# Kernel tuning notes

Measured on AMD Instinct MI355X. Metric: run time of the kernel, lower is better.

## Reference

```python
import jax, jax.numpy as jnp
import numpy as np


def setup_inputs() -> dict:
    key = jax.random.key(0)
    ks = jax.random.split(key, 10)
    B, C, D, H, W = 2, 512, 8, 32, 32
    Ck = C // 4  # shared KV head dim (and fixed query dim per intended MQA math)
    s = 0.02
    return {
        "x": jax.random.normal(ks[0], (B, C, D, H, W), dtype=jnp.float32),
        "Wq": jax.random.normal(ks[1], (Ck, C), dtype=jnp.float32) * s,
        "bq": jnp.zeros((Ck,), dtype=jnp.float32),
        "Wk": jax.random.normal(ks[2], (Ck, C), dtype=jnp.float32) * s,
        "bk": jnp.zeros((Ck,), dtype=jnp.float32),
        "Wv": jax.random.normal(ks[3], (Ck, C), dtype=jnp.float32) * s,
        "bv": jnp.zeros((Ck,), dtype=jnp.float32),
        "Wo": jax.random.normal(ks[4], (C, C), dtype=jnp.float32) * s,
        "bo": jnp.zeros((C,), dtype=jnp.float32),
    }


def reference(x, Wq, bq, Wk, bk, Wv, bv, Wo, bo):
    B, C, D, H, W = x.shape
    N = D * H * W
    Ck = Wk.shape[0]  # C // 4
    xf = x.reshape(B, C, N)  # flatten spatial dims -> sequence axis
    # 1x1 Conv3d == per-voxel linear projection over channels
    q = jnp.einsum('oc,bcn->bno', Wq, xf) + bq  # [B, N, Ck]
    k = jnp.einsum('oc,bcn->bno', Wk, xf) + bk  # [B, N, Ck]
    v = jnp.einsum('oc,bcn->bno', Wv, xf) + bv  # [B, N, Ck]
    scale = jnp.asarray(Ck, x.dtype) ** -0.5
    attn = jax.nn.softmax(jnp.einsum('bnc,bmc->bnm', q, k) * scale, axis=-1)  # [B, N, N]
    out = jnp.einsum('bnm,bmc->bnc', attn, v)  # [B, N, Ck]
    out = jnp.tile(out, (1, 1, 4))  # repeat(1,1,4) -> [B, N, C]
    out = jnp.einsum('oc,bnc->bon', Wo, out) + bo[None, :, None]  # [B, C, N]
    return out.reshape(B, C, D, H, W) + x
```

## Files before the change

kernel.cpp:

```cpp
#include <hip/hip_runtime.h>
#include <hip/hip_bf16.h>

typedef __bf16 bf16;
typedef __bf16 bf16x8 __attribute__((ext_vector_type(8)));
typedef __bf16 bf16x4 __attribute__((ext_vector_type(4)));
typedef float  f32x4  __attribute__((ext_vector_type(4)));
typedef float  f32x16 __attribute__((ext_vector_type(16)));
typedef unsigned int u32;
typedef u32 u32x4 __attribute__((ext_vector_type(4)));

constexpr int BB = 2, C = 512, NN = 8192, CK = 128;

__device__ __forceinline__ u32 cvt_pk_bf16(float lo, float hi) {
    u32 r;
    asm("v_cvt_pk_bf16_f32 %0, %1, %2" : "=v"(r) : "v"(lo), "v"(hi));
    return r;
}
__device__ __forceinline__ void pl32_swap(u32& a, u32& b) {
    asm("v_permlane32_swap_b32 %0, %1" : "+v"(a), "+v"(b));
}

__global__ __launch_bounds__(256) void k_qkv(
    const float* __restrict__ x,
    const float* __restrict__ Wq, const float* __restrict__ bq,
    const float* __restrict__ Wk, const float* __restrict__ bk,
    const float* __restrict__ Wv, const float* __restrict__ bv,
    bf16* __restrict__ qkv_ws)
{
    const int t = threadIdx.x;
    const int lane = t & 63, w = t >> 6;
    const int lr = lane & 15, lg = lane >> 4;

    const int lin = blockIdx.x;
    const int rid = (lin & 7) * 48 + (lin >> 3);
    const int n0 = (rid / 6) * 128;
    const int sub = rid % 6;
    const int which = sub >> 1;
    const int b = sub & 1;

    const float* W    = which == 0 ? Wq : (which == 1 ? Wk : Wv);
    const float* bias = which == 0 ? bq : (which == 1 ? bk : bv);
    bf16* out = qkv_ws + (size_t)which * BB * NN * CK;

    __shared__ __align__(16) char s_xT[128 * 144];
    __shared__ __align__(16) char s_w [128 * 144];

    f32x4 acc[2][8];
#pragma unroll
    for (int m = 0; m < 2; m++)
#pragma unroll
        for (int j = 0; j < 8; j++) acc[m][j] = (f32x4){0.f, 0.f, 0.f, 0.f};

    const float* xb = x + (size_t)b * C * NN;

    const int tok4 = (t & 31) * 4;
    const int c8   = (t >> 5) * 8;
    const int ob   = t >> 2;
    const int c16  = (t & 3) * 16;

    for (int kt = 0; kt < C; kt += 64) {
        __syncthreads();
        {
            float4 v[8];
#pragma unroll
            for (int i = 0; i < 8; i++)
                v[i] = *(const float4*)(xb + (size_t)(kt + c8 + i) * NN + n0 + tok4);
#pragma unroll
            for (int j = 0; j < 4; j++) {
                int tok = tok4 + j;
                bf16x8 pk = { (bf16)v[0].x, (bf16)v[1].x, (bf16)v[2].x, (bf16)v[3].x,
                              (bf16)v[4].x, (bf16)v[5].x, (bf16)v[6].x, (bf16)v[7].x };
                if (j == 1) pk = (bf16x8){ (bf16)v[0].y, (bf16)v[1].y, (bf16)v[2].y, (bf16)v[3].y,
                                           (bf16)v[4].y, (bf16)v[5].y, (bf16)v[6].y, (bf16)v[7].y };
                if (j == 2) pk = (bf16x8){ (bf16)v[0].z, (bf16)v[1].z, (bf16)v[2].z, (bf16)v[3].z,
                                           (bf16)v[4].z, (bf16)v[5].z, (bf16)v[6].z, (bf16)v[7].z };
                if (j == 3) pk = (bf16x8){ (bf16)v[0].w, (bf16)v[1].w, (bf16)v[2].w, (bf16)v[3].w,
                                           (bf16)v[4].w, (bf16)v[5].w, (bf16)v[6].w, (bf16)v[7].w };
                int off = tok * 144 + ((c8 * 2) ^ ((((tok >> 2) & 7)) << 4));
                *(bf16x8*)(s_xT + off) = pk;
            }
        }
#pragma unroll
        for (int p = 0; p < 2; p++) {
            int o = ob + p * 64;
            const float* wp = W + (size_t)o * C + kt + c16;
            float4 a0 = *(const float4*)(wp);
            float4 a1 = *(const float4*)(wp + 4);
            float4 a2 = *(const float4*)(wp + 8);
            float4 a3 = *(const float4*)(wp + 12);
            bf16x8 p0 = { (bf16)a0.x, (bf16)a0.y, (bf16)a0.z, (bf16)a0.w,
                          (bf16)a1.x, (bf16)a1.y, (bf16)a1.z, (bf16)a1.w };
            bf16x8 p1 = { (bf16)a2.x, (bf16)a2.y, (bf16)a2.z, (bf16)a2.w,
                          (bf16)a3.x, (bf16)a3.y, (bf16)a3.z, (bf16)a3.w };
            int perm = ((o >> 2) & 7) << 4;
            *(bf16x8*)(s_w + o * 144 + ((c16 * 2) ^ perm)) = p0;
            *(bf16x8*)(s_w + o * 144 + ((c16 * 2 + 16) ^ perm)) = p1;
        }
        __syncthreads();
#pragma unroll
        for (int ks = 0; ks < 2; ks++) {
            bf16x8 af[2];
#pragma unroll
            for (int m = 0; m < 2; m++) {
                int row = w * 32 + m * 16 + lr;
                af[m] = *(const bf16x8*)(s_xT + row * 144 + ((ks * 64 + lg * 16) ^ ((((row >> 2) & 7)) << 4)));
            }
#pragma unroll
            for (int j = 0; j < 8; j++) {
                int row = j * 16 + lr;
                bf16x8 bfr = *(const bf16x8*)(s_w + row * 144 + ((ks * 64 + lg * 16) ^ ((((row >> 2) & 7)) << 4)));
                acc[0][j] = __builtin_amdgcn_mfma_f32_16x16x32_bf16(af[0], bfr, acc[0][j], 0, 0, 0);
                acc[1][j] = __builtin_amdgcn_mfma_f32_16x16x32_bf16(af[1], bfr, acc[1][j], 0, 0, 0);
            }
        }
    }
#pragma unroll
    for (int m = 0; m < 2; m++)
#pragma unroll
        for (int j = 0; j < 8; j++) {
            int o = j * 16 + lr;
            float bia = bias[o];
#pragma unroll
            for (int r = 0; r < 4; r++) {
                int tok = n0 + w * 32 + m * 16 + lg * 4 + r;
                out[((size_t)b * NN + tok) * CK + o] = (bf16)(acc[m][j][r] + bia);
            }
        }
}

__global__ __launch_bounds__(512, 2) void k_attn(
    const bf16* __restrict__ qkv_ws,
    bf16* __restrict__ Opart, float* __restrict__ Lw,
    int nsplit)
{
    const int t = threadIdx.x;
    const int lane = t & 63, w = t >> 6;
    const int lq = lane & 31, hi = lane >> 5;
    const int phase = (w >> 2) & 1;

    const int total = 32 * BB * nsplit;
    const int chunkv = total >> 3;
    const int lin = blockIdx.x;
    const int rid = (lin & 7) * chunkv + (lin >> 3);
    const int qt = rid & 31;
    const int bs = rid >> 5;
    const int b = bs & 1, split = bs >> 1;

    const int q0 = qt * 256;
    const int kbeg = split * (NN / nsplit);
    const int nt = (NN / nsplit) / 64;

    const bf16* kg = qkv_ws + (size_t)BB * NN * CK;
    const bf16* vg = qkv_ws + (size_t)2 * BB * NN * CK;

    __shared__ __align__(16) char s_k[2][64 * 256];
    __shared__ __align__(16) char s_vt[3][128 * 128];

    const int kb0 = lq * 256 + ((((lq & 7) ^ hi)) << 4);
    int vbs[4];
#pragma unroll
    for (int db = 0; db < 4; db++) {
        int d = db * 32 + lq;
        vbs[db] = d * 128 + (((((d ^ (d >> 3)) & 7) ^ hi)) << 4);
    }
    const int t2 = t & 255;
    const int sc = t2 & 15, sr = t2 >> 4;
    const int kw_base = (sr * 256 + sc * 16) ^ ((sr & 7) << 4);
    const int vw_base = (sc * 1024 + sr * 8) ^ ((sc & 7) << 4);

    bf16x8 qf[8];
    {
        const float qs = 0.08838834764831845f * 1.4426950408889634f;
        const bf16* qp = qkv_ws + ((size_t)b * NN + q0 + w * 32 + lq) * CK + hi * 8;
#pragma unroll
        for (int ks = 0; ks < 8; ks++) {
            bf16x8 v = *(const bf16x8*)(qp + ks * 16);
#pragma unroll
            for (int i = 0; i < 8; i++) qf[ks][i] = (bf16)((float)v[i] * qs);
        }
    }

    f32x16 oacc[4];
#pragma unroll
    for (int db = 0; db < 4; db++)
#pragma unroll
        for (int i = 0; i < 16; i++) oacc[db][i] = 0.f;
    float lrun = 0.f;

    const bf16* kp = kg + ((size_t)b * NN + kbeg + sr) * CK + sc * 8;
    const bf16* vp = vg + ((size_t)b * NN + kbeg + sr * 4) * CK + sc * 8;
    bf16x8 stg[4];

    auto issue_loads = [&]() {
        if (w < 4) {
#pragma unroll
            for (int p = 0; p < 4; p++) stg[p] = *(const bf16x8*)(kp + (size_t)(16 * p) * CK);
        } else {
#pragma unroll
            for (int p = 0; p < 4; p++) stg[p] = *(const bf16x8*)(vp + (size_t)p * CK);
        }
        kp += (size_t)64 * CK;
        vp += (size_t)64 * CK;
    };

    auto write_lds = [&](int kbuf, int vbuf) {
        if (w < 4) {
            char* skw = s_k[kbuf] + kw_base;
#pragma unroll
            for (int p = 0; p < 4; p++)
                *(bf16x8*)(skw + p * 4096) = stg[p];
        } else {
            char* svw = s_vt[vbuf];
#pragma unroll
            for (int i = 0; i < 8; i++) {
                bf16x4 pk = { stg[0][i], stg[1][i], stg[2][i], stg[3][i] };
                *(bf16x4*)(svw + (vw_base ^ (i * 144))) = pk;
            }
        }
    };

    f32x16 sa0, sa1;
    auto do_qkt = [&](const char* sk) {
#pragma unroll
        for (int i = 0; i < 16; i++) { sa0[i] = 0.f; sa1[i] = 0.f; }
#pragma unroll
        for (int ks = 0; ks < 8; ks++) {
            bf16x8 kf0 = *(const bf16x8*)(sk + (kb0 ^ (ks * 32)));
            bf16x8 kf1 = *(const bf16x8*)(sk + ((kb0 ^ (ks * 32)) + 8192));
            sa0 = __builtin_amdgcn_mfma_f32_32x32x16_bf16(kf0, qf[ks], sa0, 0, 0, 0);
            sa1 = __builtin_amdgcn_mfma_f32_32x32x16_bf16(kf1, qf[ks], sa1, 0, 0, 0);
        }
    };

    u32 W0[8], W1[8];
    auto do_softmax = [&]() {
        f32x16 p0, p1;
#pragma unroll
        for (int i = 0; i < 16; i++) { p0[i] = exp2f(sa0[i]); p1[i] = exp2f(sa1[i]); }
        float s0 = ((p0[0] + p0[1]) + (p0[2] + p0[3])) + ((p0[4] + p0[5]) + (p0[6] + p0[7]));
        float s1 = ((p0[8] + p0[9]) + (p0[10] + p0[11])) + ((p0[12] + p0[13]) + (p0[14] + p0[15]));
        float s2 = ((p1[0] + p1[1]) + (p1[2] + p1[3])) + ((p1[4] + p1[5]) + (p1[6] + p1[7]));
        float s3 = ((p1[8] + p1[9]) + (p1[10] + p1[11])) + ((p1[12] + p1[13]) + (p1[14] + p1[15]));
        lrun += (s0 + s1) + (s2 + s3);
#pragma unroll
        for (int j = 0; j < 8; j++) {
            W0[j] = cvt_pk_bf16(p0[2 * j], p0[2 * j + 1]);
            W1[j] = cvt_pk_bf16(p1[2 * j], p1[2 * j + 1]);
        }
        pl32_swap(W0[0], W0[2]); pl32_swap(W0[1], W0[3]);
        pl32_swap(W0[4], W0[6]); pl32_swap(W0[5], W0[7]);
        pl32_swap(W1[0], W1[2]); pl32_swap(W1[1], W1[3]);
        pl32_swap(W1[4], W1[6]); pl32_swap(W1[5], W1[7]);
    };

    auto do_pv = [&](const char* sv) {
#pragma unroll
        for (int s = 0; s < 4; s++) {
            u32x4 fw;
            if (s == 0)      fw = (u32x4){W0[0], W0[1], W0[2], W0[3]};
            else if (s == 1) fw = (u32x4){W0[4], W0[5], W0[6], W0[7]};
            else if (s == 2) fw = (u32x4){W1[0], W1[1], W1[2], W1[3]};
            else             fw = (u32x4){W1[4], W1[5], W1[6], W1[7]};
            bf16x8 pa = __builtin_bit_cast(bf16x8, fw);
            const int coff = (s >> 1) * 64 + (s & 1) * 32;
#pragma unroll
            for (int db = 0; db < 4; db++) {
                bf16x8 vf = *(const bf16x8*)(sv + (vbs[db] ^ coff));
                oacc[db] = __builtin_amdgcn_mfma_f32_32x32x16_bf16(pa, vf, oacc[db], 0, 0, 0);
            }
        }
    };

    issue_loads();
    write_lds(0, 0);
    __syncthreads();
    if (nt > 1) issue_loads();
    __builtin_amdgcn_s_setprio(1);
    do_qkt(s_k[0]);
    __builtin_amdgcn_s_setprio(0);
    if (!phase) do_softmax();

    int vb_w = 1, vb_r = 0;
    for (int it = 1; it < nt; it++) {
        write_lds(it & 1, vb_w);
        __syncthreads();
        if (it + 1 < nt) issue_loads();
        if (phase) do_softmax();
        __builtin_amdgcn_s_setprio(1);
        do_qkt(s_k[it & 1]);
        do_pv(s_vt[vb_r]);
        __builtin_amdgcn_s_setprio(0);
        if (!phase) do_softmax();
        vb_r = vb_w;
        vb_w = vb_w + 1 == 3 ? 0 : vb_w + 1;
    }
    if (phase) do_softmax();
    __builtin_amdgcn_s_setprio(1);
    do_pv(s_vt[vb_r]);
    __builtin_amdgcn_s_setprio(0);

    size_t obase = (((size_t)split * BB + b) * NN + q0 + w * 32);
    float ls = lrun + __shfl_xor(lrun, 32);
    if (lane < 32) {
        Lw[obase + lq] = ls;
    }
#pragma unroll
    for (int r = 0; r < 16; r++) {
        int qrow = (r & 3) + 8 * (r >> 2) + 4 * hi;
        bf16* op = Opart + (obase + qrow) * CK + lq;
#pragma unroll
        for (int db = 0; db < 4; db++) op[db * 32] = (bf16)oacc[db][r];
    }
}

__global__ __launch_bounds__(256) void k_out(
    const float* __restrict__ x, const float* __restrict__ Wo, const float* __restrict__ bo,
    const bf16* __restrict__ Opart, const float* __restrict__ Lw,
    float* __restrict__ y, int nsplit)
{
    const int t = threadIdx.x;
    const int lane = t & 63, w = t >> 6;
    const int lr = lane & 15, lg = lane >> 4;
    const int n0 = blockIdx.x * 128;
    const int o0 = blockIdx.y * 64;
    const int b = blockIdx.z;

    __shared__ __align__(16) char s_w[64 * 256];
    __shared__ __align__(16) char s_a[128 * 256];
    __shared__ float s_linv[128];

    if (t < 128) {
        int row = n0 + t;
        float L = 0.f;
        for (int s = 0; s < nsplit; s++)
            L += Lw[((size_t)s * BB + b) * NN + row];
        s_linv[t] = 1.f / L;
    }
    {
        int c4 = (t & 31) * 4, rbase = t >> 5;
#pragma unroll
        for (int p = 0; p < 8; p++) {
            int row = rbase + p * 8;
            const float* wp = Wo + (size_t)(o0 + row) * C + c4;
            float4 a0 = *(const float4*)(wp);
            float4 a1 = *(const float4*)(wp + 128);
            float4 a2 = *(const float4*)(wp + 256);
            float4 a3 = *(const float4*)(wp + 384);
            bf16x4 r4 = { (bf16)(a0.x + a1.x + a2.x + a3.x), (bf16)(a0.y + a1.y + a2.y + a3.y),
                          (bf16)(a0.z + a1.z + a2.z + a3.z), (bf16)(a0.w + a1.w + a2.w + a3.w) };
            int off = (row * 256 + c4 * 2) ^ ((row & 7) << 4);
            *(bf16x4*)(s_w + off) = r4;
        }
    }
    __syncthreads();
    {
        int chunk = t & 15, rbase = t >> 4;
#pragma unroll
        for (int p = 0; p < 8; p++) {
            int row = rbase + p * 16;
            float accv[8];
#pragma unroll
            for (int i = 0; i < 8; i++) accv[i] = 0.f;
            for (int s = 0; s < nsplit; s++) {
                const bf16* op = Opart + (((size_t)s * BB + b) * NN + n0 + row) * CK + chunk * 8;
                bf16x8 v = *(const bf16x8*)op;
#pragma unroll
                for (int i = 0; i < 8; i++) accv[i] += (float)v[i];
            }
            float inv = s_linv[row];
            bf16x8 outv;
#pragma unroll
            for (int i = 0; i < 8; i++) outv[i] = (bf16)(accv[i] * inv);
            int off = (row * 256 + chunk * 16) ^ ((row & 7) << 4);
            *(bf16x8*)(s_a + off) = outv;
        }
    }
    __syncthreads();

    f32x4 acc[8];
#pragma unroll
    for (int j = 0; j < 8; j++) acc[j] = (f32x4){0.f, 0.f, 0.f, 0.f};
#pragma unroll
    for (int ks = 0; ks < 4; ks++) {
        int row = w * 16 + lr;
        int aoff = (row * 256 + (ks * 32 + lg * 8) * 2) ^ ((row & 7) << 4);
        bf16x8 wf = *(const bf16x8*)(s_w + aoff);
#pragma unroll
        for (int j = 0; j < 8; j++) {
            int nrow = j * 16 + lr;
            int boff = (nrow * 256 + (ks * 32 + lg * 8) * 2) ^ ((nrow & 7) << 4);
            bf16x8 af = *(const bf16x8*)(s_a + boff);
            acc[j] = __builtin_amdgcn_mfma_f32_16x16x32_bf16(wf, af, acc[j], 0, 0, 0);
        }
    }
#pragma unroll
    for (int j = 0; j < 8; j++) {
        int n = n0 + j * 16 + lr;
#pragma unroll
        for (int r = 0; r < 4; r++) {
            int o = o0 + w * 16 + lg * 4 + r;
            size_t idx = ((size_t)b * C + o) * NN + n;
            y[idx] = acc[j][r] + bo[o] + x[idx];
        }
    }
}

extern "C" void kernel_launch(void* const* d_in, const int* in_sizes, int n_in,
                              void* d_out, int out_size, void* d_ws, size_t ws_size,
                              hipStream_t stream)
{
    const float* x  = (const float*)d_in[0];
    const float* Wq = (const float*)d_in[1];
    const float* bq = (const float*)d_in[2];
    const float* Wk = (const float*)d_in[3];
    const float* bk = (const float*)d_in[4];
    const float* Wv = (const float*)d_in[5];
    const float* bv = (const float*)d_in[6];
    const float* Wo = (const float*)d_in[7];
    const float* bo = (const float*)d_in[8];
    float* y = (float*)d_out;

    const size_t qkv_elems = (size_t)3 * BB * NN * CK;

    bf16* qkv = (bf16*)d_ws;
    bf16* Opart = qkv + qkv_elems;

    int nsplit = 4;
    {
        size_t fixed = qkv_elems * sizeof(bf16);
        size_t per_split = (size_t)BB * NN * CK * sizeof(bf16) + (size_t)BB * NN * sizeof(float);
        while (nsplit > 1 && fixed + (size_t)nsplit * per_split > ws_size) nsplit >>= 1;
    }
    float* Lw = (float*)(Opart + (size_t)nsplit * BB * NN * CK);

    k_qkv<<<dim3(384, 1, 1), 256, 0, stream>>>(x, Wq, bq, Wk, bk, Wv, bv, qkv);
    k_attn<<<dim3(32 * BB * nsplit, 1, 1), 512, 0, stream>>>(qkv, Opart, Lw, nsplit);
    k_out<<<dim3(NN / 128, C / 64, BB), 256, 0, stream>>>(x, Wo, bo, Opart, Lw, y, nsplit);
}
```

Before: 134.7 us.

## Double key tile to 128 and drop phase-staggered softmax pipeline in attention

The attention kernel now processes 128 keys per iteration instead of 64. It doubles the K and transposed-V LDS buffers and doubles the register staging. V is transposed into 256-byte rows with a new swizzle, and the triple-buffered V ring becomes double buffering. The old scheme staggered softmax between wave groups across iterations. It is replaced by a straight sequence of two QK^T halves, two softmaxes, and then two PV passes per tile. This halves the barrier count per key but gives up the cross-wave overlap of softmax with MFMA. LDS use and register pressure rise, which may hurt occupancy at 2 blocks per CU.

```diff
diff --git a/kernel.cpp b/kernel.cpp
--- a/kernel.cpp
+++ b/kernel.cpp
@@ -136,7 +136,6 @@
     const int t = threadIdx.x;
     const int lane = t & 63, w = t >> 6;
     const int lq = lane & 31, hi = lane >> 5;
-    const int phase = (w >> 2) & 1;
 
     const int total = 32 * BB * nsplit;
     const int chunkv = total >> 3;
@@ -148,25 +147,24 @@
 
     const int q0 = qt * 256;
     const int kbeg = split * (NN / nsplit);
-    const int nt = (NN / nsplit) / 64;
+    const int nt = (NN / nsplit) / 128;
 
     const bf16* kg = qkv_ws + (size_t)BB * NN * CK;
     const bf16* vg = qkv_ws + (size_t)2 * BB * NN * CK;
 
-    __shared__ __align__(16) char s_k[2][64 * 256];
-    __shared__ __align__(16) char s_vt[3][128 * 128];
+    __shared__ __align__(16) char s_k[2][128 * 256];
+    __shared__ __align__(16) char s_vt[2][128 * 256];
 
     const int kb0 = lq * 256 + ((((lq & 7) ^ hi)) << 4);
     int vbs[4];
 #pragma unroll
     for (int db = 0; db < 4; db++) {
         int d = db * 32 + lq;
-        vbs[db] = d * 128 + (((((d ^ (d >> 3)) & 7) ^ hi)) << 4);
+        vbs[db] = d * 256 + (((d ^ (d >> 3)) & 7) << 4);
     }
     const int t2 = t & 255;
     const int sc = t2 & 15, sr = t2 >> 4;
     const int kw_base = (sr * 256 + sc * 16) ^ ((sr & 7) << 4);
-    const int vw_base = (sc * 1024 + sr * 8) ^ ((sc & 7) << 4);
 
     bf16x8 qf[8];
     {
@@ -188,52 +186,54 @@
     float lrun = 0.f;
 
     const bf16* kp = kg + ((size_t)b * NN + kbeg + sr) * CK + sc * 8;
-    const bf16* vp = vg + ((size_t)b * NN + kbeg + sr * 4) * CK + sc * 8;
-    bf16x8 stg[4];
+    const bf16* vp = vg + ((size_t)b * NN + kbeg + sr * 8) * CK + sc * 8;
+    bf16x8 stg[8];
 
     auto issue_loads = [&]() {
         if (w < 4) {
 #pragma unroll
-            for (int p = 0; p < 4; p++) stg[p] = *(const bf16x8*)(kp + (size_t)(16 * p) * CK);
+            for (int p = 0; p < 8; p++) stg[p] = *(const bf16x8*)(kp + (size_t)(16 * p) * CK);
         } else {
 #pragma unroll
-            for (int p = 0; p < 4; p++) stg[p] = *(const bf16x8*)(vp + (size_t)p * CK);
-        }
-        kp += (size_t)64 * CK;
-        vp += (size_t)64 * CK;
+            for (int j = 0; j < 8; j++) stg[j] = *(const bf16x8*)(vp + (size_t)j * CK);
+        }
+        kp += (size_t)128 * CK;
+        vp += (size_t)128 * CK;
     };
 
-    auto write_lds = [&](int kbuf, int vbuf) {
+    auto write_lds = [&](int buf) {
         if (w < 4) {
-            char* skw = s_k[kbuf] + kw_base;
-#pragma unroll
-            for (int p = 0; p < 4; p++)
+            char* skw = s_k[buf] + kw_base;
+#pragma unroll
+            for (int p = 0; p < 8; p++)
                 *(bf16x8*)(skw + p * 4096) = stg[p];
         } else {
-            char* svw = s_vt[vbuf];
+            char* svw = s_vt[buf];
 #pragma unroll
             for (int i = 0; i < 8; i++) {
-                bf16x4 pk = { stg[0][i], stg[1][i], stg[2][i], stg[3][i] };
-                *(bf16x4*)(svw + (vw_base ^ (i * 144))) = pk;
+                bf16x8 pk = { stg[0][i], stg[1][i], stg[2][i], stg[3][i],
+                              stg[4][i], stg[5][i], stg[6][i], stg[7][i] };
+                int d = sc * 8 + i;
+                *(bf16x8*)(svw + d * 256 + ((sr * 16) ^ (((i ^ (sc & 7)) & 7) << 4))) = pk;
             }
         }
     };
 
     f32x16 sa0, sa1;
-    auto do_qkt = [&](const char* sk) {
+    auto do_qkt = [&](const char* sk, int h) {
 #pragma unroll
         for (int i = 0; i < 16; i++) { sa0[i] = 0.f; sa1[i] = 0.f; }
+        const char* skh = sk + h * 16384;
 #pragma unroll
         for (int ks = 0; ks < 8; ks++) {
-            bf16x8 kf0 = *(const bf16x8*)(sk + (kb0 ^ (ks * 32)));
-            bf16x8 kf1 = *(const bf16x8*)(sk + ((kb0 ^ (ks * 32)) + 8192));
+            bf16x8 kf0 = *(const bf16x8*)(skh + (kb0 ^ (ks * 32)));
+            bf16x8 kf1 = *(const bf16x8*)(skh + ((kb0 ^ (ks * 32)) + 8192));
             sa0 = __builtin_amdgcn_mfma_f32_32x32x16_bf16(kf0, qf[ks], sa0, 0, 0, 0);
             sa1 = __builtin_amdgcn_mfma_f32_32x32x16_bf16(kf1, qf[ks], sa1, 0, 0, 0);
         }
     };
 
-    u32 W0[8], W1[8];
-    auto do_softmax = [&]() {
+    auto do_softmax = [&](u32* Wa, u32* Wb) {
         f32x16 p0, p1;
 #pragma unroll
         for (int i = 0; i < 16; i++) { p0[i] = exp2f(sa0[i]); p1[i] = exp2f(sa1[i]); }
@@ -244,60 +244,57 @@
         lrun += (s0 + s1) + (s2 + s3);
 #pragma unroll
         for (int j = 0; j < 8; j++) {
-            W0[j] = cvt_pk_bf16(p0[2 * j], p0[2 * j + 1]);
-            W1[j] = cvt_pk_bf16(p1[2 * j], p1[2 * j + 1]);
-        }
-        pl32_swap(W0[0], W0[2]); pl32_swap(W0[1], W0[3]);
-        pl32_swap(W0[4], W0[6]); pl32_swap(W0[5], W0[7]);
-        pl32_swap(W1[0], W1[2]); pl32_swap(W1[1], W1[3]);
-        pl32_swap(W1[4], W1[6]); pl32_swap(W1[5], W1[7]);
+            Wa[j] = cvt_pk_bf16(p0[2 * j], p0[2 * j + 1]);
+            Wb[j] = cvt_pk_bf16(p1[2 * j], p1[2 * j + 1]);
+        }
+        pl32_swap(Wa[0], Wa[2]); pl32_swap(Wa[1], Wa[3]);
+        pl32_swap(Wa[4], Wa[6]); pl32_swap(Wa[5], Wa[7]);
+        pl32_swap(Wb[0], Wb[2]); pl32_swap(Wb[1], Wb[3]);
+        pl32_swap(Wb[4], Wb[6]); pl32_swap(Wb[5], Wb[7]);
     };
 
-    auto do_pv = [&](const char* sv) {
+    auto do_pv = [&](const char* sv, const u32* Wa, const u32* Wb, int h) {
 #pragma unroll
         for (int s = 0; s < 4; s++) {
             u32x4 fw;
-            if (s == 0)      fw = (u32x4){W0[0], W0[1], W0[2], W0[3]};
-            else if (s == 1) fw = (u32x4){W0[4], W0[5], W0[6], W0[7]};
-            else if (s == 2) fw = (u32x4){W1[0], W1[1], W1[2], W1[3]};
-            else             fw = (u32x4){W1[4], W1[5], W1[6], W1[7]};
+            if (s == 0)      fw = (u32x4){Wa[0], Wa[1], Wa[2], Wa[3]};
+            else if (s == 1) fw = (u32x4){Wa[4], Wa[5], Wa[6], Wa[7]};
+            else if (s == 2) fw = (u32x4){Wb[0], Wb[1], Wb[2], Wb[3]};
+            else             fw = (u32x4){Wb[4], Wb[5], Wb[6], Wb[7]};
             bf16x8 pa = __builtin_bit_cast(bf16x8, fw);
-            const int coff = (s >> 1) * 64 + (s & 1) * 32;
+            const int keybyte = h * 128 + s * 32 + hi * 16;
 #pragma unroll
             for (int db = 0; db < 4; db++) {
-                bf16x8 vf = *(const bf16x8*)(sv + (vbs[db] ^ coff));
+                bf16x8 vf = *(const bf16x8*)(sv + (vbs[db] ^ keybyte));
                 oacc[db] = __builtin_amdgcn_mfma_f32_32x32x16_bf16(pa, vf, oacc[db], 0, 0, 0);
             }
         }
     };
 
     issue_loads();
-    write_lds(0, 0);
-    __syncthreads();
-    if (nt > 1) issue_loads();
-    __builtin_amdgcn_s_setprio(1);
-    do_qkt(s_k[0]);
-    __builtin_amdgcn_s_setprio(0);
-    if (!phase) do_softmax();
-
-    int vb_w = 1, vb_r = 0;
-    for (int it = 1; it < nt; it++) {
-        write_lds(it & 1, vb_w);
+    u32 W0[8], W1[8], W2[8], W3[8];
+
+    for (int it = 0; it < nt; it++) {
+        const int buf = it & 1;
+        write_lds(buf);
         __syncthreads();
         if (it + 1 < nt) issue_loads();
-        if (phase) do_softmax();
+        const char* sk = s_k[buf];
+        const char* sv = s_vt[buf];
+
         __builtin_amdgcn_s_setprio(1);
-        do_qkt(s_k[it & 1]);
-        do_pv(s_vt[vb_r]);
+        do_qkt(sk, 0);
         __builtin_amdgcn_s_setprio(0);
-        if (!phase) do_softmax();
-        vb_r = vb_w;
-        vb_w = vb_w + 1 == 3 ? 0 : vb_w + 1;
-    }
-    if (phase) do_softmax();
-    __builtin_amdgcn_s_setprio(1);
-    do_pv(s_vt[vb_r]);
-    __builtin_amdgcn_s_setprio(0);
+        do_softmax(W0, W1);
+        __builtin_amdgcn_s_setprio(1);
+        do_qkt(sk, 1);
+        __builtin_amdgcn_s_setprio(0);
+        do_softmax(W2, W3);
+        __builtin_amdgcn_s_setprio(1);
+        do_pv(sv, W0, W1, 0);
+        do_pv(sv, W2, W3, 1);
+        __builtin_amdgcn_s_setprio(0);
+    }
 
     size_t obase = (((size_t)split * BB + b) * NN + q0 + w * 32);
     float ls = lrun + __shfl_xor(lrun, 32);
```

After: 186.6 us. 1.39x slower.
